# Kernel tuning notes

Measured on AMD Instinct MI355X. Metric: run time of the kernel, lower is better.

Reference implementation:

```python
import jax, jax.numpy as jnp
import numpy as np

B, C, H, G1, G2 = 16, 64, 128, 64, 64  # batch, input channels, hidden, grid dims


def setup_inputs() -> dict:
    key = jax.random.key(0)
    ks = jax.random.split(key, 5)
    s = 0.05  # small init to keep gates in a sane range
    return {
        "x": jax.random.normal(ks[0], (B, C, G1, G2), jnp.float32),
        "W_ih": jax.random.normal(ks[1], (2, 4 * H, C), jnp.float32) * s,
        "W_hh": jax.random.normal(ks[2], (2, 4 * H, 2 * H), jnp.float32) * s,
        "b_ih": jax.random.normal(ks[3], (2, 4 * H), jnp.float32) * s,
        "b_hh": jax.random.normal(ks[4], (2, 4 * H), jnp.float32) * s,
    }


def _lstm_update(gates, c_prev):
    # PyTorch LSTMCell gate order: i, f, g, o
    i, f, g, o = jnp.split(gates, 4, axis=-1)
    c = jax.nn.sigmoid(f) * c_prev + jax.nn.sigmoid(i) * jnp.tanh(g)
    h = jax.nn.sigmoid(o) * jnp.tanh(c)
    return h, c


def _grid_lstm(x, W_ih, W_hh, b_ih, b_hh):
    Bn = x.shape[0]
    Hn = W_hh.shape[1] // 4
    g2 = x.shape[3]
    # Precompute the input contribution to the gates for every grid location
    # (no recurrence on x). xg: [2(dim), G1, G2, B, 4H]
    xg = jnp.einsum('bcij,dgc->dijbg', x, W_ih) \
        + (b_ih + b_hh)[:, None, None, None, :]
    Wh0t = W_hh[0].T  # [2H, 4H]
    Wh1t = W_hh[1].T  # [2H, 4H]
    z = jnp.zeros((Bn, Hn), x.dtype)
    zrow = jnp.zeros((g2, Bn, Hn), x.dtype)

    def col_step(carry, xs):
        # recurrence along grid dim 1 (columns)
        h2, c2 = carry                # dim-1 state from (i, j-1): [B, H]
        xg0, xg1, h1p, c1p = xs       # dim-0 state from (i-1, j)
        Hcat = jnp.concatenate([h1p, h2], axis=-1)  # [B, 2H] shared hidden
        h1n, c1n = _lstm_update(xg0 + Hcat @ Wh0t, c1p)
        h2n, c2n = _lstm_update(xg1 + Hcat @ Wh1t, c2)
        return (h2n, c2n), (h1n, c1n, h2n)

    def row_step(carry, xg_row):
        # recurrence along grid dim 0 (rows); carry = dim-0 state of prev row
        h1_row, c1_row = carry        # [G2, B, H]
        _, (h1s, c1s, h2s) = jax.lax.scan(
            col_step, (z, z), (xg_row[0], xg_row[1], h1_row, c1_row))
        return (h1s, c1s), (h1s, h2s)

    xg_rows = jnp.moveaxis(xg, 1, 0)  # [G1, 2, G2, B, 4H]
    _, (h1_all, h2_all) = jax.lax.scan(row_step, (zrow, zrow), xg_rows)
    # h*_all: [G1, G2, B, H]; concat hidden of all dims along channel
    out = jnp.concatenate([h1_all, h2_all], axis=-1)  # [G1, G2, B, 2H]
    return out.transpose(2, 3, 0, 1)                  # [B, 2H, G1, G2]


def reference(x, W_ih, W_hh, b_ih, b_hh):
    return _grid_lstm(x, W_ih, W_hh, b_ih, b_hh)
```

## Files before the change

kernel.cpp:

```cpp
#include <hip/hip_runtime.h>
#include <math.h>

namespace {

constexpr int BN = 16;
constexpr int CN = 64;
constexpr int HN = 128;
constexpr int GN = 64;
constexpr int KH = 2 * HN;
constexpr int KTOT = KH + CN;
constexpr int LDSK = 328;
constexpr int GBS2 = 260;

typedef _Float16 half8 __attribute__((ext_vector_type(8)));
typedef float float4v __attribute__((ext_vector_type(4)));
typedef unsigned long long u64;

__device__ __forceinline__ float fsig(float z) {
    return 1.f / (1.f + expf(-z));
}

__global__ __launch_bounds__(64) void wprep_kernel(
    const float* __restrict__ Wih,
    const float* __restrict__ Whh,
    _Float16* __restrict__ wf)
{
    const int blk = blockIdx.x;
    const int nt = blk / 10, ks = blk - nt * 10;
    const int lane = threadIdx.x;
    const int dd = nt >> 5;
    const int gr = (nt & 31) * 16 + (lane & 15);
    const int k0 = ks * 32 + (lane >> 4) * 8;
    _Float16* dst = wf + ((size_t)blk * 64 + lane) * 8;
    #pragma unroll
    for (int e = 0; e < 8; ++e) {
        const int k = k0 + e;
        const float v = (k < KH)
            ? Whh[((size_t)(dd * 512 + gr)) * KH + k]
            : Wih[((size_t)(dd * 512 + gr)) * CN + (k - KH)];
        dst[e] = (_Float16)v;
    }
}

__global__ __launch_bounds__(256) void xconv_kernel(
    const float* __restrict__ x, _Float16* __restrict__ xb)
{
    __shared__ float tile[CN][GN + 1];
    const int b = blockIdx.x >> 6;
    const int i = blockIdx.x & 63;
    const int t = threadIdx.x;
    const int tj = t & 63, tc = t >> 6;
    for (int c0 = 0; c0 < CN; c0 += 4) {
        const int c = c0 + tc;
        tile[c][tj] = x[((size_t)(b * CN + c) * GN + i) * GN + tj];
    }
    __syncthreads();
    const int wc = t & 63, wj = t >> 6;
    for (int j0 = 0; j0 < GN; j0 += 4) {
        const int j = j0 + wj;
        xb[((size_t)(i * GN + j) * BN + b) * CN + wc] = (_Float16)tile[wc][j];
    }
}

__global__ __launch_bounds__(256) void out_kernel(
    const _Float16* __restrict__ hbuf, float* __restrict__ out)
{
    const int b = blockIdx.x >> 6;
    const int i = blockIdx.x & 63;
    const int t = threadIdx.x;
    float* op = out + ((size_t)(b * KH + t)) * (GN * GN) + (size_t)i * GN;
    const _Float16* hp = hbuf + ((size_t)i * GN * BN + b) * KH + t;
    #pragma unroll 4
    for (int j = 0; j < GN; ++j)
        op[j] = (float)hp[(size_t)j * (BN * KH)];
}

template <bool USE_XB>
__global__ __launch_bounds__(512, 1) void grid_lstm_rowq(
    const _Float16* __restrict__ wf,
    const _Float16* __restrict__ xb,
    const float* __restrict__ x,
    const float* __restrict__ bih,
    const float* __restrict__ bhh,
    _Float16* __restrict__ hbuf,
    float* __restrict__ cmail,
    int* __restrict__ flag1,
    int* __restrict__ flag2)
{
    __shared__ __align__(16) _Float16 Wl2[16 * 8 * 64 * 8];
    __shared__ __align__(16) _Float16 Hc[BN * LDSK];
    __shared__ __align__(16) float gb[BN * GBS2];
    __shared__ float blds[256];

    const int blk = blockIdx.x;
    const int i  = blk >> 2;
    const int s  = blk & 3;
    const int dd = s >> 1;
    const int ub = s & 1;

    const int t = threadIdx.x;
    const int lane = t & 63;
    const int wv = t >> 6;
    const int l15 = lane & 15;
    const int l4 = lane >> 4;

    const half8* wfv = (const half8*)wf;
    half8* wl2v = (half8*)Wl2;

    for (int e = t; e < 16 * 8 * 64; e += 512) {
        const int ln = e & 63, ks = (e >> 6) & 7, tl = e >> 9;
        const int q = tl >> 2, w = tl & 3;
        const int nt = dd * 32 + q * 8 + ub * 4 + w;
        wl2v[e] = wfv[(size_t)(nt * 10 + ks) * 64 + ln];
    }
    const int tlA = 2 * wv, tlB = 2 * wv + 1;
    const int ntA = dd * 32 + (tlA >> 2) * 8 + ub * 4 + (tlA & 3);
    const int ntB = dd * 32 + (tlB >> 2) * 8 + ub * 4 + (tlB & 3);
    const half8 wA8 = wfv[(size_t)(ntA * 10 + 8) * 64 + lane];
    const half8 wA9 = wfv[(size_t)(ntA * 10 + 9) * 64 + lane];
    const half8 wB8 = wfv[(size_t)(ntB * 10 + 8) * 64 + lane];
    const half8 wB9 = wfv[(size_t)(ntB * 10 + 9) * 64 + lane];
    if (t < 256) {
        const int q = t >> 6, uu = t & 63;
        const int gr = dd * 512 + q * 128 + ub * 64 + uu;
        blds[t] = bih[gr] + bhh[gr];
    }
    const int eb = t >> 5;
    const int u2 = (t & 31) * 2;
    float c2r0 = 0.f, c2r1 = 0.f;
    __syncthreads();

    for (int j = 0; j < GN; ++j) {
        const int cellidx = i * GN + j;

        if (t == 0 && j > 0) {
            const int* fp = flag2 + cellidx - 1;
            int it = 0;
            while (__hip_atomic_load(fp, __ATOMIC_RELAXED,
                                     __HIP_MEMORY_SCOPE_AGENT) < 2) {
                __builtin_amdgcn_s_sleep(1);
                if (++it > (1 << 24)) break;
            }
        }
        if (t == 64 && i > 0) {
            const int* fp = flag1 + cellidx - GN;
            int it = 0;
            while (__hip_atomic_load(fp, __ATOMIC_RELAXED,
                                     __HIP_MEMORY_SCOPE_AGENT) < 2) {
                __builtin_amdgcn_s_sleep(1);
                if (++it > (1 << 24)) break;
            }
        }
        __syncthreads();

        {
            const int b = t >> 5, k4 = t & 31;
            u64 v1 = 0, v2 = 0;
            if (i > 0)
                v1 = __hip_atomic_load(
                    (const u64*)(hbuf + ((size_t)(cellidx - GN)) * (BN * KH)
                                 + b * KH + k4 * 4),
                    __ATOMIC_RELAXED, __HIP_MEMORY_SCOPE_AGENT);
            if (j > 0)
                v2 = __hip_atomic_load(
                    (const u64*)(hbuf + ((size_t)(cellidx - 1)) * (BN * KH)
                                 + b * KH + HN + k4 * 4),
                    __ATOMIC_RELAXED, __HIP_MEMORY_SCOPE_AGENT);
            *(u64*)(&Hc[b * LDSK + k4 * 4]) = v1;
            *(u64*)(&Hc[b * LDSK + HN + k4 * 4]) = v2;
            if (USE_XB) {
                if (t < 256) {
                    const int b2 = t >> 4, c4 = t & 15;
                    *(u64*)(&Hc[b2 * LDSK + KH + c4 * 4]) =
                        *(const u64*)(xb + ((size_t)cellidx) * (BN * CN)
                                      + b2 * CN + c4 * 4);
                }
            } else {
                #pragma unroll
                for (int r = 0; r < 2; ++r) {
                    const int e = t + r * 512;
                    const int b2 = e >> 6, c = e & 63;
                    Hc[b2 * LDSK + KH + c] =
                        (_Float16)x[(size_t)(b2 * 64 + c) * 4096 + i * 64 + j];
                }
            }
        }
        __syncthreads();

        {
            half8 a[10];
            #pragma unroll
            for (int ks = 0; ks < 10; ++ks)
                a[ks] = *(const half8*)(&Hc[l15 * LDSK + ks * 32 + l4 * 8]);
            float4v acc0 = {0.f, 0.f, 0.f, 0.f};
            float4v acc1 = {0.f, 0.f, 0.f, 0.f};
            #pragma unroll
            for (int ks = 0; ks < 8; ++ks) {
                acc0 = __builtin_amdgcn_mfma_f32_16x16x32_f16(
                    a[ks], wl2v[(tlA * 8 + ks) * 64 + lane], acc0, 0, 0, 0);
                acc1 = __builtin_amdgcn_mfma_f32_16x16x32_f16(
                    a[ks], wl2v[(tlB * 8 + ks) * 64 + lane], acc1, 0, 0, 0);
            }
            acc0 = __builtin_amdgcn_mfma_f32_16x16x32_f16(a[8], wA8, acc0, 0, 0, 0);
            acc0 = __builtin_amdgcn_mfma_f32_16x16x32_f16(a[9], wA9, acc0, 0, 0, 0);
            acc1 = __builtin_amdgcn_mfma_f32_16x16x32_f16(a[8], wB8, acc1, 0, 0, 0);
            acc1 = __builtin_amdgcn_mfma_f32_16x16x32_f16(a[9], wB9, acc1, 0, 0, 0);
            #pragma unroll
            for (int rg = 0; rg < 4; ++rg) {
                gb[(l4 * 4 + rg) * GBS2 + tlA * 16 + l15] = acc0[rg];
                gb[(l4 * 4 + rg) * GBS2 + tlB * 16 + l15] = acc1[rg];
            }
        }
        __syncthreads();

        {
            float g0[4], g1[4];
            #pragma unroll
            for (int q = 0; q < 4; ++q) {
                g0[q] = gb[eb * GBS2 + q * 64 + u2]     + blds[q * 64 + u2];
                g1[q] = gb[eb * GBS2 + q * 64 + u2 + 1] + blds[q * 64 + u2 + 1];
            }
            const int hu = ub * 64 + u2;
            float cp0, cp1;
            if (dd == 0) {
                cp0 = 0.f; cp1 = 0.f;
                if (i > 0) {
                    const u64 cq = __hip_atomic_load(
                        (const u64*)(cmail + ((size_t)((((i - 1) & 1) * GN + j) * BN
                                     + eb)) * HN + hu),
                        __ATOMIC_RELAXED, __HIP_MEMORY_SCOPE_AGENT);
                    union { u64 q; float f[2]; } cu; cu.q = cq;
                    cp0 = cu.f[0]; cp1 = cu.f[1];
                }
            } else {
                cp0 = c2r0; cp1 = c2r1;
            }
            const float c0 = fsig(g0[1]) * cp0 + fsig(g0[0]) * tanhf(g0[2]);
            const float c1 = fsig(g1[1]) * cp1 + fsig(g1[0]) * tanhf(g1[2]);
            const float h0 = fsig(g0[3]) * tanhf(c0);
            const float h1 = fsig(g1[3]) * tanhf(c1);
            union { unsigned int u; _Float16 f[2]; } hp;
            hp.f[0] = (_Float16)h0; hp.f[1] = (_Float16)h1;

            if (dd == 0) {
                union { u64 q; float f[2]; } cn; cn.f[0] = c0; cn.f[1] = c1;
                __hip_atomic_store(
                    (u64*)(cmail + ((size_t)(((i & 1) * GN + j) * BN + eb)) * HN + hu),
                    cn.q, __ATOMIC_RELAXED, __HIP_MEMORY_SCOPE_AGENT);
            } else {
                c2r0 = c0; c2r1 = c1;
            }
            __hip_atomic_store(
                (unsigned int*)(hbuf + ((size_t)cellidx) * (BN * KH)
                                + eb * KH + dd * HN + hu),
                hp.u, __ATOMIC_RELAXED, __HIP_MEMORY_SCOPE_AGENT);
        }
        asm volatile("s_waitcnt vmcnt(0)" ::: "memory");
        __syncthreads();
        if (t == 0)
            __hip_atomic_fetch_add((dd == 0 ? flag1 : flag2) + cellidx, 1,
                                   __ATOMIC_RELAXED, __HIP_MEMORY_SCOPE_AGENT);
    }
}

constexpr int KCH = 32;
constexpr int NCH = KTOT / KCH;

__device__ __forceinline__ float sigmoidf_(float z) {
    return 1.f / (1.f + expf(-z));
}

__global__ __launch_bounds__(256, 1) void diag_kernel(
    const float* __restrict__ x, const float* __restrict__ Wih,
    const float* __restrict__ Whh, const float* __restrict__ bih,
    const float* __restrict__ bhh, float* __restrict__ out,
    float* __restrict__ cbuf, int d)
{
    __shared__ float HcF[BN][KTOT];
    __shared__ float Wch[KCH][257];
    const int cell = blockIdx.x >> 2;
    const int slice = blockIdx.x & 3;
    const int dd = slice >> 1;
    const int h0 = (slice & 1) * 64;
    const int i0 = (d > GN - 1) ? (d - (GN - 1)) : 0;
    const int i = i0 + cell;
    const int j = d - i;
    const int t = threadIdx.x;
    for (int e = t; e < BN * KTOT; e += 256) {
        const int b = e / KTOT, k = e - b * KTOT;
        float v;
        if (k < HN)      v = (i > 0) ? out[((b * KH + k) * GN + (i - 1)) * GN + j] : 0.f;
        else if (k < KH) v = (j > 0) ? out[((b * KH + k) * GN + i) * GN + (j - 1)] : 0.f;
        else             v = x[((b * CN + (k - KH)) * GN + i) * GN + j];
        HcF[b][k] = v;
    }
    const int h = t & 63, bg = t >> 6;
    const int grow = dd * 4 * HN + bg * HN + h0 + h;
    float acc[4][4];
    #pragma unroll
    for (int qq = 0; qq < 4; ++qq)
        #pragma unroll
        for (int bb = 0; bb < 4; ++bb) acc[qq][bb] = 0.f;
    for (int kb = 0; kb < NCH; ++kb) {
        const int kbase = kb * KCH;
        __syncthreads();
        const float* src = (kbase < KH) ? (Whh + (size_t)grow * KH + kbase)
                                        : (Wih + (size_t)grow * CN + (kbase - KH));
        #pragma unroll
        for (int k4 = 0; k4 < KCH / 4; ++k4) {
            const float4 w = *(const float4*)(src + k4 * 4);
            Wch[k4 * 4 + 0][t] = w.x; Wch[k4 * 4 + 1][t] = w.y;
            Wch[k4 * 4 + 2][t] = w.z; Wch[k4 * 4 + 3][t] = w.w;
        }
        __syncthreads();
        #pragma unroll 8
        for (int kk = 0; kk < KCH; ++kk) {
            const float w0 = Wch[kk][0 * 64 + h], w1 = Wch[kk][1 * 64 + h];
            const float w2 = Wch[kk][2 * 64 + h], w3 = Wch[kk][3 * 64 + h];
            #pragma unroll
            for (int bb = 0; bb < 4; ++bb) {
                const float hv = HcF[bg * 4 + bb][kbase + kk];
                acc[0][bb] = fmaf(w0, hv, acc[0][bb]);
                acc[1][bb] = fmaf(w1, hv, acc[1][bb]);
                acc[2][bb] = fmaf(w2, hv, acc[2][bb]);
                acc[3][bb] = fmaf(w3, hv, acc[3][bb]);
            }
        }
    }
    const int hu = h0 + h;
    float bias[4];
    #pragma unroll
    for (int qq = 0; qq < 4; ++qq) {
        const int gidx = dd * 4 * HN + qq * HN + hu;
        bias[qq] = bih[gidx] + bhh[gidx];
    }
    float* cptr = (dd == 0) ? (cbuf + (size_t)j * BN * HN)
                            : (cbuf + (size_t)GN * BN * HN + (size_t)i * BN * HN);
    const bool has_prev = (dd == 0) ? (i > 0) : (j > 0);
    #pragma unroll
    for (int bb = 0; bb < 4; ++bb) {
        const int b = bg * 4 + bb;
        const float gi = sigmoidf_(acc[0][bb] + bias[0]);
        const float gf = sigmoidf_(acc[1][bb] + bias[1]);
        const float gg = tanhf(acc[2][bb] + bias[2]);
        const float go = sigmoidf_(acc[3][bb] + bias[3]);
        const float cp = has_prev ? cptr[b * HN + hu] : 0.f;
        const float c = gf * cp + gi * gg;
        cptr[b * HN + hu] = c;
        out[((b * KH + dd * HN + hu) * GN + i) * GN + j] = go * tanhf(c);
    }
}

}

extern "C" void kernel_launch(void* const* d_in, const int* in_sizes, int n_in,
                              void* d_out, int out_size, void* d_ws, size_t ws_size,
                              hipStream_t stream) {
    const float* x   = (const float*)d_in[0];
    const float* Wih = (const float*)d_in[1];
    const float* Whh = (const float*)d_in[2];
    const float* bih = (const float*)d_in[3];
    const float* bhh = (const float*)d_in[4];
    float* out = (float*)d_out;

    const size_t HB_BYTES = (size_t)GN * GN * BN * KH * 2;
    const size_t WF_BYTES = (size_t)640 * 64 * 8 * 2;
    const size_t CM_BYTES = (size_t)2 * GN * BN * HN * 4;
    const size_t FL_BYTES = (size_t)GN * GN * 4;
    const size_t XB_BYTES = (size_t)GN * GN * BN * CN * 2;
    const size_t NEED_MIN  = HB_BYTES + WF_BYTES + CM_BYTES + 2 * FL_BYTES;
    const size_t NEED_FULL = NEED_MIN + XB_BYTES;

    if (ws_size >= NEED_MIN) {
        char* p = (char*)d_ws;
        _Float16* hbuf  = (_Float16*)p;                 p += HB_BYTES;
        _Float16* wfp   = (_Float16*)p;                 p += WF_BYTES;
        float*    cmail = (float*)p;                    p += CM_BYTES;
        int*      flag1 = (int*)p;                      p += FL_BYTES;
        int*      flag2 = (int*)p;                      p += FL_BYTES;
        _Float16* xbp   = (_Float16*)p;

        hipMemsetAsync(flag1, 0, 2 * FL_BYTES, stream);
        hipLaunchKernelGGL(wprep_kernel, dim3(640), dim3(64), 0, stream,
                           Wih, Whh, wfp);

        if (ws_size >= NEED_FULL) {
            hipLaunchKernelGGL(xconv_kernel, dim3(BN * GN), dim3(256), 0, stream,
                               x, xbp);
            void* args[] = { (void*)&wfp, (void*)&xbp, (void*)&x, (void*)&bih,
                             (void*)&bhh, (void*)&hbuf, (void*)&cmail,
                             (void*)&flag1, (void*)&flag2 };
            hipLaunchCooperativeKernel((const void*)grid_lstm_rowq<true>,
                                       dim3(256), dim3(512), args, 0, stream);
        } else {
            void* args[] = { (void*)&wfp, (void*)&xbp, (void*)&x, (void*)&bih,
                             (void*)&bhh, (void*)&hbuf, (void*)&cmail,
                             (void*)&flag1, (void*)&flag2 };
            hipLaunchCooperativeKernel((const void*)grid_lstm_rowq<false>,
                                       dim3(256), dim3(512), args, 0, stream);
        }
        hipLaunchKernelGGL(out_kernel, dim3(BN * GN), dim3(256), 0, stream,
                           hbuf, out);
    } else {
        float* cbuf = (float*)d_ws;
        for (int d = 0; d < 2 * GN - 1; ++d) {
            const int i0 = (d > GN - 1) ? (d - (GN - 1)) : 0;
            const int i1 = (d < GN - 1) ? d : (GN - 1);
            const int nc = i1 - i0 + 1;
            hipLaunchKernelGGL(diag_kernel, dim3(nc * 4), dim3(256), 0, stream,
                               x, Wih, Whh, bih, bhh, out, cbuf, d);
        }
    }
}
```

Before: 508.6 us.

## Split dependency waits per half-block, prefetch next x slice, merge prep kernels

Two half-blocks now handle the wait and load for each recurrence dependency. One waits on the row above (h1) and the other on the left neighbour (h2), in place of one thread waiting on both and then a block-wide barrier. The x input slice for the next cell is loaded during the gate math of the current cell, which takes it off the critical path. The weight-prep and x-conversion kernels are merged into one launch, and the block-to-row mapping is changed so the four blocks of a row sit in different parts of the grid. The aim is lower per-cell sync latency and launch overhead, at the cost of more concurrent spinning threads and a changed CU placement.

```diff
diff --git a/kernel.cpp b/kernel.cpp
--- a/kernel.cpp
+++ b/kernel.cpp
@@ -20,45 +20,49 @@
     return 1.f / (1.f + expf(-z));
 }
 
-__global__ __launch_bounds__(64) void wprep_kernel(
+__global__ __launch_bounds__(256) void prep_kernel(
     const float* __restrict__ Wih,
     const float* __restrict__ Whh,
-    _Float16* __restrict__ wf)
+    _Float16* __restrict__ wf,
+    const float* __restrict__ x,
+    _Float16* __restrict__ xb)
 {
     const int blk = blockIdx.x;
-    const int nt = blk / 10, ks = blk - nt * 10;
-    const int lane = threadIdx.x;
-    const int dd = nt >> 5;
-    const int gr = (nt & 31) * 16 + (lane & 15);
-    const int k0 = ks * 32 + (lane >> 4) * 8;
-    _Float16* dst = wf + ((size_t)blk * 64 + lane) * 8;
-    #pragma unroll
-    for (int e = 0; e < 8; ++e) {
-        const int k = k0 + e;
-        const float v = (k < KH)
-            ? Whh[((size_t)(dd * 512 + gr)) * KH + k]
-            : Wih[((size_t)(dd * 512 + gr)) * CN + (k - KH)];
-        dst[e] = (_Float16)v;
-    }
-}
-
-__global__ __launch_bounds__(256) void xconv_kernel(
-    const float* __restrict__ x, _Float16* __restrict__ xb)
-{
-    __shared__ float tile[CN][GN + 1];
-    const int b = blockIdx.x >> 6;
-    const int i = blockIdx.x & 63;
-    const int t = threadIdx.x;
-    const int tj = t & 63, tc = t >> 6;
-    for (int c0 = 0; c0 < CN; c0 += 4) {
-        const int c = c0 + tc;
-        tile[c][tj] = x[((size_t)(b * CN + c) * GN + i) * GN + tj];
-    }
-    __syncthreads();
-    const int wc = t & 63, wj = t >> 6;
-    for (int j0 = 0; j0 < GN; j0 += 4) {
-        const int j = j0 + wj;
-        xb[((size_t)(i * GN + j) * BN + b) * CN + wc] = (_Float16)tile[wc][j];
+    if (blk < 640) {
+        const int t = threadIdx.x;
+        if (t < 64) {
+            const int nt = blk / 10, ks = blk - nt * 10;
+            const int lane = t;
+            const int dd = nt >> 5;
+            const int gr = (nt & 31) * 16 + (lane & 15);
+            const int k0 = ks * 32 + (lane >> 4) * 8;
+            _Float16* dst = wf + ((size_t)blk * 64 + lane) * 8;
+            #pragma unroll
+            for (int e = 0; e < 8; ++e) {
+                const int k = k0 + e;
+                const float v = (k < KH)
+                    ? Whh[((size_t)(dd * 512 + gr)) * KH + k]
+                    : Wih[((size_t)(dd * 512 + gr)) * CN + (k - KH)];
+                dst[e] = (_Float16)v;
+            }
+        }
+    } else {
+        __shared__ float tile[CN][GN + 1];
+        const int bb = blk - 640;
+        const int b = bb >> 6;
+        const int i = bb & 63;
+        const int t = threadIdx.x;
+        const int tj = t & 63, tc = t >> 6;
+        for (int c0 = 0; c0 < CN; c0 += 4) {
+            const int c = c0 + tc;
+            tile[c][tj] = x[((size_t)(b * CN + c) * GN + i) * GN + tj];
+        }
+        __syncthreads();
+        const int wc = t & 63, wj = t >> 6;
+        for (int j0 = 0; j0 < GN; j0 += 4) {
+            const int j = j0 + wj;
+            xb[((size_t)(i * GN + j) * BN + b) * CN + wc] = (_Float16)tile[wc][j];
+        }
     }
 }
 
@@ -93,8 +97,8 @@
     __shared__ float blds[256];
 
     const int blk = blockIdx.x;
-    const int i  = blk >> 2;
-    const int s  = blk & 3;
+    const int i  = blk & 63;
+    const int s  = blk >> 6;
     const int dd = s >> 1;
     const int ub = s & 1;
 
@@ -125,64 +129,71 @@
         const int gr = dd * 512 + q * 128 + ub * 64 + uu;
         blds[t] = bih[gr] + bhh[gr];
     }
+    const int sb = (t & 255) >> 4;
+    const int sk = (t & 15);
+    const bool roleH1 = (t < 256);
     const int eb = t >> 5;
     const int u2 = (t & 31) * 2;
     float c2r0 = 0.f, c2r1 = 0.f;
+
+    if (USE_XB) {
+        if (t < 256)
+            *(u64*)(&Hc[(t >> 4) * LDSK + KH + (t & 15) * 4]) =
+                *(const u64*)(xb + ((size_t)(i * GN)) * (BN * CN)
+                              + (t >> 4) * CN + (t & 15) * 4);
+    } else {
+        #pragma unroll
+        for (int r = 0; r < 2; ++r) {
+            const int e = t + r * 512;
+            const int b2 = e >> 6, c = e & 63;
+            Hc[b2 * LDSK + KH + c] =
+                (_Float16)x[(size_t)(b2 * 64 + c) * 4096 + i * 64];
+        }
+    }
     __syncthreads();
 
     for (int j = 0; j < GN; ++j) {
         const int cellidx = i * GN + j;
 
-        if (t == 0 && j > 0) {
-            const int* fp = flag2 + cellidx - 1;
-            int it = 0;
-            while (__hip_atomic_load(fp, __ATOMIC_RELAXED,
-                                     __HIP_MEMORY_SCOPE_AGENT) < 2) {
-                __builtin_amdgcn_s_sleep(1);
-                if (++it > (1 << 24)) break;
-            }
-        }
-        if (t == 64 && i > 0) {
-            const int* fp = flag1 + cellidx - GN;
-            int it = 0;
-            while (__hip_atomic_load(fp, __ATOMIC_RELAXED,
-                                     __HIP_MEMORY_SCOPE_AGENT) < 2) {
-                __builtin_amdgcn_s_sleep(1);
-                if (++it > (1 << 24)) break;
-            }
-        }
-        __syncthreads();
-
         {
-            const int b = t >> 5, k4 = t & 31;
-            u64 v1 = 0, v2 = 0;
-            if (i > 0)
-                v1 = __hip_atomic_load(
-                    (const u64*)(hbuf + ((size_t)(cellidx - GN)) * (BN * KH)
-                                 + b * KH + k4 * 4),
-                    __ATOMIC_RELAXED, __HIP_MEMORY_SCOPE_AGENT);
-            if (j > 0)
-                v2 = __hip_atomic_load(
-                    (const u64*)(hbuf + ((size_t)(cellidx - 1)) * (BN * KH)
-                                 + b * KH + HN + k4 * 4),
-                    __ATOMIC_RELAXED, __HIP_MEMORY_SCOPE_AGENT);
-            *(u64*)(&Hc[b * LDSK + k4 * 4]) = v1;
-            *(u64*)(&Hc[b * LDSK + HN + k4 * 4]) = v2;
-            if (USE_XB) {
-                if (t < 256) {
-                    const int b2 = t >> 4, c4 = t & 15;
-                    *(u64*)(&Hc[b2 * LDSK + KH + c4 * 4]) =
-                        *(const u64*)(xb + ((size_t)cellidx) * (BN * CN)
-                                      + b2 * CN + c4 * 4);
+            u64 q0 = 0, q1 = 0;
+            if (roleH1) {
+                if (i > 0) {
+                    const int* fp = flag1 + cellidx - GN;
+                    int it = 0;
+                    while (__hip_atomic_load(fp, __ATOMIC_RELAXED,
+                                             __HIP_MEMORY_SCOPE_AGENT) < 2) {
+                        __builtin_amdgcn_s_sleep(1);
+                        if (++it > (1 << 24)) break;
+                    }
+                    const u64* src = (const u64*)(hbuf
+                        + ((size_t)(cellidx - GN)) * (BN * KH) + sb * KH + sk * 8);
+                    q0 = __hip_atomic_load(src, __ATOMIC_RELAXED,
+                                           __HIP_MEMORY_SCOPE_AGENT);
+                    q1 = __hip_atomic_load(src + 1, __ATOMIC_RELAXED,
+                                           __HIP_MEMORY_SCOPE_AGENT);
                 }
+                *(u64*)(&Hc[sb * LDSK + sk * 8]) = q0;
+                *(u64*)(&Hc[sb * LDSK + sk * 8 + 4]) = q1;
             } else {
-                #pragma unroll
-                for (int r = 0; r < 2; ++r) {
-                    const int e = t + r * 512;
-                    const int b2 = e >> 6, c = e & 63;
-                    Hc[b2 * LDSK + KH + c] =
-                        (_Float16)x[(size_t)(b2 * 64 + c) * 4096 + i * 64 + j];
+                if (j > 0) {
+                    const int* fp = flag2 + cellidx - 1;
+                    int it = 0;
+                    while (__hip_atomic_load(fp, __ATOMIC_RELAXED,
+                                             __HIP_MEMORY_SCOPE_AGENT) < 2) {
+                        __builtin_amdgcn_s_sleep(1);
+                        if (++it > (1 << 24)) break;
+                    }
+                    const u64* src = (const u64*)(hbuf
+                        + ((size_t)(cellidx - 1)) * (BN * KH)
+                        + sb * KH + HN + sk * 8);
+                    q0 = __hip_atomic_load(src, __ATOMIC_RELAXED,
+                                           __HIP_MEMORY_SCOPE_AGENT);
+                    q1 = __hip_atomic_load(src + 1, __ATOMIC_RELAXED,
+                                           __HIP_MEMORY_SCOPE_AGENT);
                 }
+                *(u64*)(&Hc[sb * LDSK + HN + sk * 8]) = q0;
+                *(u64*)(&Hc[sb * LDSK + HN + sk * 8 + 4]) = q1;
             }
         }
         __syncthreads();
@@ -212,6 +223,12 @@
             }
         }
         __syncthreads();
+
+        u64 xv = 0;
+        const bool doX = USE_XB && (t < 256) && (j + 1 < GN);
+        if (doX)
+            xv = *(const u64*)(xb + ((size_t)(cellidx + 1)) * (BN * CN)
+                               + (t >> 4) * CN + (t & 15) * 4);
 
         {
             float g0[4], g1[4];
@@ -255,6 +272,19 @@
                                 + eb * KH + dd * HN + hu),
                 hp.u, __ATOMIC_RELAXED, __HIP_MEMORY_SCOPE_AGENT);
         }
+
+        if (doX)
+            *(u64*)(&Hc[(t >> 4) * LDSK + KH + (t & 15) * 4]) = xv;
+        if (!USE_XB && (j + 1 < GN)) {
+            #pragma unroll
+            for (int r = 0; r < 2; ++r) {
+                const int e = t + r * 512;
+                const int b2 = e >> 6, c = e & 63;
+                Hc[b2 * LDSK + KH + c] =
+                    (_Float16)x[(size_t)(b2 * 64 + c) * 4096 + i * 64 + (j + 1)];
+            }
+        }
+
         asm volatile("s_waitcnt vmcnt(0)" ::: "memory");
         __syncthreads();
         if (t == 0)
@@ -381,18 +411,18 @@
         _Float16* xbp   = (_Float16*)p;
 
         hipMemsetAsync(flag1, 0, 2 * FL_BYTES, stream);
-        hipLaunchKernelGGL(wprep_kernel, dim3(640), dim3(64), 0, stream,
-                           Wih, Whh, wfp);
 
         if (ws_size >= NEED_FULL) {
-            hipLaunchKernelGGL(xconv_kernel, dim3(BN * GN), dim3(256), 0, stream,
-                               x, xbp);
+            hipLaunchKernelGGL(prep_kernel, dim3(640 + BN * GN), dim3(256), 0,
+                               stream, Wih, Whh, wfp, x, xbp);
             void* args[] = { (void*)&wfp, (void*)&xbp, (void*)&x, (void*)&bih,
                              (void*)&bhh, (void*)&hbuf, (void*)&cmail,
                              (void*)&flag1, (void*)&flag2 };
             hipLaunchCooperativeKernel((const void*)grid_lstm_rowq<true>,
                                        dim3(256), dim3(512), args, 0, stream);
         } else {
+            hipLaunchKernelGGL(prep_kernel, dim3(640), dim3(256), 0,
+                               stream, Wih, Whh, wfp, x, xbp);
             void* args[] = { (void*)&wfp, (void*)&xbp, (void*)&x, (void*)&bih,
                              (void*)&bhh, (void*)&hbuf, (void*)&cmail,
                              (void*)&flag1, (void*)&flag2 };
```

Result: faster. 467.4 us (-8.1%).
